# Kernel optimization log

Hardware: AMD Instinct MI355X
Metric: run time of the kernel (lower is better)

## Reference

```python
import jax, jax.numpy as jnp
import numpy as np

S = 8192      # total packed tokens
H = 1152      # hidden size
NH = 16       # heads
HD = 72       # head dim
NSEG = 8      # number of packed (equal-length) sequences
L = S // NSEG # tokens per sequence
SCALE = HD ** -0.5


def setup_inputs() -> dict:
    key = jax.random.key(0)
    ks = jax.random.split(key, 4)
    hidden_states = jax.random.normal(ks[0], (1, S, H), jnp.float32)
    # Real rotary cos/sin per token position within each sequence.
    inv_freq = 1.0 / (10000.0 ** (np.arange(0, HD, 2, dtype=np.float64) / HD))
    freqs = np.outer(np.arange(L, dtype=np.float64), inv_freq)  # [L, HD/2]
    emb = np.concatenate([freqs, freqs], axis=-1)               # [L, HD]
    cos = jnp.asarray(np.tile(np.cos(emb), (NSEG, 1)), jnp.float32)  # [S, HD]
    sin = jnp.asarray(np.tile(np.sin(emb), (NSEG, 1)), jnp.float32)
    Wqkv = jax.random.normal(ks[1], (H, 3 * H), jnp.float32) * (H ** -0.5)
    bqkv = jnp.zeros((3 * H,), jnp.float32)
    Wout = jax.random.normal(ks[2], (H, H), jnp.float32) * (H ** -0.5)
    bout = jnp.zeros((H,), jnp.float32)
    cu_seqlens = jnp.arange(NSEG + 1, dtype=jnp.int32) * L
    return dict(hidden_states=hidden_states, cos=cos, sin=sin,
                Wqkv=Wqkv, bqkv=bqkv, Wout=Wout, bout=bout,
                cu_seqlens=cu_seqlens)


def _rotate_half(x):
    return jnp.concatenate([-x[..., HD // 2:], x[..., :HD // 2]], axis=-1)


def reference(hidden_states, cos, sin, Wqkv, bqkv, Wout, bout, cu_seqlens):
    # QKV projection (fused)
    qkv = hidden_states @ Wqkv + bqkv                 # [1, S, 3H]
    q, k, v = jnp.split(qkv, [H, 2 * H], axis=-1)
    q = q.reshape(1, S, NH, HD)
    k = k.reshape(1, S, NH, HD)
    v = v.reshape(1, S, NH, HD)
    # Inline RoPE on q/k (cos/sin broadcast over heads)
    c = cos[None, :, None, :]
    s = sin[None, :, None, :]
    q = q * c + _rotate_half(q) * s
    k = k * c + _rotate_half(k) * s
    # Varlen (block-diagonal) non-causal attention: equal-length segments
    q = q.reshape(NSEG, L, NH, HD)
    k = k.reshape(NSEG, L, NH, HD)
    v = v.reshape(NSEG, L, NH, HD)
    scores = jnp.einsum('nqhd,nkhd->nhqk', q, k) * SCALE  # [NSEG, NH, L, L]
    probs = jax.nn.softmax(scores, axis=-1)
    ctx = jnp.einsum('nhqk,nkhd->nqhd', probs, v)         # [NSEG, L, NH, HD]
    ctx = ctx.reshape(1, S, H)
    # Output projection
    return ctx @ Wout + bout
```

## Files before the change

kernel.cpp:

```cpp
#include <hip/hip_runtime.h>
#include <hip/hip_fp16.h>
#include <cstdint>

typedef _Float16 half8 __attribute__((ext_vector_type(8)));
typedef _Float16 half4 __attribute__((ext_vector_type(4)));
typedef float floatx4 __attribute__((ext_vector_type(4)));

#define S_TOT 8192
#define H_DIM 1152
#define NHEAD 16
#define HD 72
#define QSTR 96
#define KSTR 104
#define PSTR 76
#define VSTR 76
#define VT_TILE 6080
#define NSEG 8
#define SEGL 1024
#define QSCALE 0.17002324631230988f

__device__ __forceinline__ void gld_lds16(const void* g, void* l) {
  __builtin_amdgcn_global_load_lds((const __attribute__((address_space(1))) void*)g,
                                   (__attribute__((address_space(3))) void*)l, 16, 0, 0);
}

__global__ void cast_f32_f16(const float* __restrict__ in, _Float16* __restrict__ out, int n) {
  int i = (blockIdx.x * 256 + threadIdx.x) * 4;
  if (i < n) {
    float4 v = *(const float4*)(in + i);
    half4 o = { (_Float16)v.x, (_Float16)v.y, (_Float16)v.z, (_Float16)v.w };
    *(half4*)(out + i) = o;
  }
}

__global__ void transpose_cast(const float* __restrict__ W, _Float16* __restrict__ Wt,
                               int R, int C) {
  __shared__ float tile[32][33];
  int tx = threadIdx.x, ty = threadIdx.y;
  int bx = blockIdx.x, by = blockIdx.y;
#pragma unroll
  for (int i = 0; i < 4; ++i)
    tile[ty + i * 8][tx] = W[(size_t)(by * 32 + ty + i * 8) * C + bx * 32 + tx];
  __syncthreads();
#pragma unroll
  for (int i = 0; i < 4; ++i)
    Wt[(size_t)(bx * 32 + ty + i * 8) * R + by * 32 + tx] = (_Float16)tile[tx][ty + i * 8];
}

template <bool OUT_HALF>
__global__ __launch_bounds__(512, 2) void gemm256(
    const _Float16* __restrict__ A, const _Float16* __restrict__ Bt,
    const float* __restrict__ bias, float* __restrict__ Cf, _Float16* __restrict__ Ch,
    int M, int N, int K, int NT) {
  extern __shared__ half8 smem8[];
  char* smem = (char*)smem8;
  const int tid = threadIdx.x;
  const int lane = tid & 63;
  const int w = tid >> 6;
  const int quad = lane >> 4, l16 = lane & 15;
  const int wm = w >> 2, wn = w & 3;

  const int orig = blockIdx.x;
  const int xcd = orig & 7, widx = orig >> 3;
  const int mt = xcd * 4 + (widx & 3), nt = widx >> 2;
  const int m0 = mt * 256, n0 = nt * 256;

  const _Float16* pA[2];
  const _Float16* pB[2];
#pragma unroll
  for (int i = 0; i < 2; ++i) {
    int c = i * 512 + tid;
    int r = c >> 2, cs = c & 3;
    int col = ((cs ^ ((r >> 1) & 3)) << 3);
    pA[i] = A + (size_t)(m0 + r) * K + col;
    int br = n0 + r; if (br >= N) br = N - 1;
    pB[i] = Bt + (size_t)br * K + col;
  }
  const int st0 = tid * 16, st1 = tid * 16 + 8192;
  const int rsl = ((quad ^ ((l16 >> 1) & 3)) << 4);
  const int aoff = (wm * 128 + l16) * 64 + rsl;
  const int boff = 16384 + (wn * 64 + l16) * 64 + rsl;

  half8 afA[8], bfA[4], afB[8], bfB[4];
  floatx4 acc[8][4] = {};

#define STG_A(ds, kcol) { \
  gld_lds16(pA[0] + (kcol), smem + (ds) * 32768 + st0); \
  gld_lds16(pA[1] + (kcol), smem + (ds) * 32768 + st1); }
#define STG_B(ds, kcol) { \
  gld_lds16(pB[0] + (kcol), smem + (ds) * 32768 + 16384 + st0); \
  gld_lds16(pB[1] + (kcol), smem + (ds) * 32768 + 16384 + st1); }
#define LDB4(s, bfx) { \
  _Pragma("unroll") for (int in = 0; in < 4; ++in) \
    bfx[in] = *(const half8*)(smem + (s) * 32768 + boff + in * 1024); }
#define LDA8(s, afx) { \
  _Pragma("unroll") for (int j = 0; j < 8; ++j) \
    afx[j] = *(const half8*)(smem + (s) * 32768 + aoff + j * 1024); }
#define MFMA32(afx, bfx) { \
  __builtin_amdgcn_s_setprio(1); \
  _Pragma("unroll") for (int j = 0; j < 8; ++j) \
  _Pragma("unroll") for (int in = 0; in < 4; ++in) \
    acc[j][in] = \
      __builtin_amdgcn_mfma_f32_16x16x32_f16(afx[j], bfx[in], acc[j][in], 0, 0, 0); \
  __builtin_amdgcn_s_setprio(0); }
#define BAR() __builtin_amdgcn_s_barrier()
#define SBAR() __builtin_amdgcn_sched_barrier(0)
#define LGKM0() { asm volatile("s_waitcnt lgkmcnt(0)" ::: "memory"); SBAR(); }
#define VMWAIT(t) { \
  if ((t) + 3 < KT)        { asm volatile("s_waitcnt vmcnt(4)" ::: "memory"); } \
  else if ((t) + 3 == KT)  { asm volatile("s_waitcnt vmcnt(0)" ::: "memory"); } }

  STG_A(0, 0);  STG_B(0, 0);
  STG_A(1, 32); STG_B(1, 32);
  STG_A(2, 64); STG_B(2, 64);
  asm volatile("s_waitcnt vmcnt(4)" ::: "memory");
  BAR();
  LDB4(0, bfA); LDA8(0, afA);
  LGKM0();

  const int KT = K >> 5;
#pragma unroll 1
  for (int u = 0; u < KT; u += 2) {
    {
      const int rs = (u + 1) & 3, ws = (u + 3) & 3;
      LDB4(rs, bfB); LDA8(rs, afB);
      if (u + 3 < KT) { STG_A(ws, (u + 3) * 32); STG_B(ws, (u + 3) * 32); }
      SBAR();
      MFMA32(afA, bfA);
      SBAR();
      LGKM0();
      VMWAIT(u);
      BAR();
    }
    {
      const int rs = (u + 2) & 3, ws = (u + 4) & 3;
      if (u + 2 < KT) { LDB4(rs, bfA); LDA8(rs, afA); }
      if (u + 4 < KT) { STG_A(ws, (u + 4) * 32); STG_B(ws, (u + 4) * 32); }
      SBAR();
      MFMA32(afB, bfB);
      SBAR();
      LGKM0();
      VMWAIT(u + 1);
      if (u + 2 < KT) BAR();
    }
  }
#undef STG_A
#undef STG_B
#undef LDB4
#undef LDA8
#undef MFMA32
#undef BAR
#undef SBAR
#undef LGKM0
#undef VMWAIT

#pragma unroll
  for (int im = 0; im < 8; ++im) {
    int m = m0 + wm * 128 + im * 16 + quad * 4;
#pragma unroll
    for (int in = 0; in < 4; ++in) {
      int n = n0 + wn * 64 + in * 16 + l16;
      if (n < N) {
        float b = bias[n];
#pragma unroll
        for (int r = 0; r < 4; ++r) {
          float v = acc[im][in][r] + b;
          if (OUT_HALF) Ch[(size_t)(m + r) * N + n] = (_Float16)v;
          else          Cf[(size_t)(m + r) * N + n] = v;
        }
      }
    }
  }
}

template <bool OUT_HALF>
__global__ __launch_bounds__(256) void gemm_bt(
    const _Float16* __restrict__ A, const _Float16* __restrict__ Bt,
    const float* __restrict__ bias, float* __restrict__ Cf, _Float16* __restrict__ Ch,
    int M, int N, int K, int NT) {
  __shared__ __align__(16) _Float16 As[128 * 72];
  __shared__ __align__(16) _Float16 Bs[128 * 72];
  const int tid = threadIdx.x;
  const int lane = tid & 63, w = tid >> 6;
  const int quad = lane >> 4, l16 = lane & 15;
  const int wm = w >> 1, wn = w & 1;
  const int id = blockIdx.x;
  const int j = id & 7, k = id >> 3;
  const int nt_ = k % NT, mt_ = (k / NT) * 8 + j;
  const int m0 = mt_ * 128, n0 = nt_ * 128;

  int rowi[5], cci[5];
#pragma unroll
  for (int i = 0; i < 5; ++i) {
    int c = tid + i * 256;
    int r = c / 9, cc = c - r * 9;
    rowi[i] = r;
    cci[i] = (cc == 8) ? 0 : cc;
  }

  floatx4 acc[4][4] = {};

  for (int kt = 0; kt < K; kt += 64) {
    __syncthreads();
#pragma unroll
    for (int i = 0; i < 4; ++i) {
      gld_lds16(A + (size_t)(m0 + rowi[i]) * K + kt + cci[i] * 8, (char*)As + (tid + i * 256) * 16);
      gld_lds16(Bt + (size_t)(n0 + rowi[i]) * K + kt + cci[i] * 8, (char*)Bs + (tid + i * 256) * 16);
    }
    if (tid < 128) {
      gld_lds16(A + (size_t)(m0 + rowi[4]) * K + kt + cci[4] * 8, (char*)As + (tid + 1024) * 16);
      gld_lds16(Bt + (size_t)(n0 + rowi[4]) * K + kt + cci[4] * 8, (char*)Bs + (tid + 1024) * 16);
    }
    __syncthreads();
#pragma unroll
    for (int kk = 0; kk < 2; ++kk) {
      half8 af[4], bf[4];
#pragma unroll
      for (int im = 0; im < 4; ++im)
        af[im] = *(const half8*)&As[(wm * 64 + im * 16 + l16) * 72 + kk * 32 + quad * 8];
#pragma unroll
      for (int in = 0; in < 4; ++in)
        bf[in] = *(const half8*)&Bs[(wn * 64 + in * 16 + l16) * 72 + kk * 32 + quad * 8];
#pragma unroll
      for (int im = 0; im < 4; ++im)
#pragma unroll
        for (int in = 0; in < 4; ++in)
          acc[im][in] = __builtin_amdgcn_mfma_f32_16x16x32_f16(af[im], bf[in], acc[im][in], 0, 0, 0);
    }
  }
#pragma unroll
  for (int im = 0; im < 4; ++im) {
    int m = m0 + wm * 64 + im * 16 + quad * 4;
#pragma unroll
    for (int in = 0; in < 4; ++in) {
      int n = n0 + wn * 64 + in * 16 + l16;
      float b = bias[n];
#pragma unroll
      for (int r = 0; r < 4; ++r) {
        float v = acc[im][in][r] + b;
        if (OUT_HALF) Ch[(size_t)(m + r) * N + n] = (_Float16)v;
        else          Cf[(size_t)(m + r) * N + n] = v;
      }
    }
  }
}

__global__ __launch_bounds__(256) void rope_scatter(
    const _Float16* __restrict__ QKV,
    const float* __restrict__ cosb,
    const float* __restrict__ sinb,
    _Float16* __restrict__ Qo, _Float16* __restrict__ Ko) {
  __shared__ __align__(16) _Float16 Ls[256 * 120];
  const int tid = threadIdx.x;
  const int t0 = blockIdx.x * 256;
  const int t = t0 + tid;
  const int l = t & 1023, h = (t >> 10) & 15, n = t >> 14;
  const int s = n * SEGL + l;
  const _Float16* q = QKV + (size_t)s * 3456 + h * HD;
  const _Float16* k = q + H_DIM;
  const float* cs = cosb + (size_t)s * HD;
  const float* sn = sinb + (size_t)s * HD;
  half8 z = {};
  {
    _Float16 qr[72], qv[72];
#pragma unroll
    for (int i = 0; i < 9; ++i) *(half8*)&qr[8 * i] = *(const half8*)(q + 8 * i);
#pragma unroll
    for (int d = 0; d < 36; ++d) {
      float c0 = cs[d], s0 = sn[d], c1 = cs[d + 36], s1 = sn[d + 36];
      float a = (float)qr[d], b = (float)qr[d + 36];
      qv[d]      = (_Float16)((a * c0 - b * s0) * QSCALE);
      qv[d + 36] = (_Float16)((b * c1 + a * s1) * QSCALE);
    }
#pragma unroll
    for (int i = 0; i < 9; ++i) *(half8*)&Ls[tid * 104 + 8 * i] = *(half8*)&qv[8 * i];
#pragma unroll
    for (int i = 9; i < 12; ++i) *(half8*)&Ls[tid * 104 + 8 * i] = z;
  }
  __syncthreads();
  {
    _Float16* dst = Qo + (size_t)t0 * QSTR;
#pragma unroll
    for (int it = 0; it < 12; ++it) {
      int j = tid + it * 256;
      int row = j / 12, c = j - row * 12;
      *(half8*)(dst + (size_t)j * 8) = *(const half8*)&Ls[row * 104 + c * 8];
    }
  }
  __syncthreads();
  {
    _Float16 kr[72], kv[72];
#pragma unroll
    for (int i = 0; i < 9; ++i) *(half8*)&kr[8 * i] = *(const half8*)(k + 8 * i);
#pragma unroll
    for (int d = 0; d < 36; ++d) {
      float c0 = cs[d], s0 = sn[d], c1 = cs[d + 36], s1 = sn[d + 36];
      float a = (float)kr[d], b = (float)kr[d + 36];
      kv[d]      = (_Float16)(a * c0 - b * s0);
      kv[d + 36] = (_Float16)(b * c1 + a * s1);
    }
#pragma unroll
    for (int i = 0; i < 9; ++i) *(half8*)&Ls[tid * 120 + 8 * i] = *(half8*)&kv[8 * i];
#pragma unroll
    for (int i = 9; i < 13; ++i) *(half8*)&Ls[tid * 120 + 8 * i] = z;
  }
  __syncthreads();
  {
    _Float16* dst = Ko + (size_t)t0 * KSTR;
#pragma unroll
    for (int it = 0; it < 13; ++it) {
      int j = tid + it * 256;
      int row = j / 13, c = j - row * 13;
      *(half8*)(dst + (size_t)j * 8) = *(const half8*)&Ls[row * 120 + c * 8];
    }
  }
}

__global__ __launch_bounds__(256) void transpose_v(const _Float16* __restrict__ QKV,
                                                   _Float16* __restrict__ Vt) {
  __shared__ __align__(16) _Float16 Vs[64 * 88];
  const int tid = threadIdx.x;
  const int kb = blockIdx.x, h = blockIdx.y, n = blockIdx.z;
  const int s0 = n * SEGL + kb * 64;
  const _Float16* src = QKV + (size_t)s0 * 3456 + 2 * H_DIM + h * HD;
  for (int idx = tid; idx < 576; idx += 256) {
    int key = idx / 9, c = idx - key * 9;
    *(half8*)&Vs[key * 88 + c * 8] = *(const half8*)(src + (size_t)key * 3456 + c * 8);
  }
  __syncthreads();
  _Float16* dst = Vt + (((size_t)(n * NHEAD + h)) * 16 + kb) * VT_TILE;
  for (int idx = tid; idx < 800; idx += 256) {
    int d = idx / 10, c = idx - d * 10;
    if (c < 8) {
      half8 v = {};
      if (d < HD) {
#pragma unroll
        for (int j = 0; j < 8; ++j) v[j] = Vs[(c * 8 + j) * 88 + d];
      } else if (d == HD) {
#pragma unroll
        for (int j = 0; j < 8; ++j) v[j] = (_Float16)1.0f;
      }
      *(half8*)(dst + d * VSTR + c * 8) = v;
    } else if (c == 8) {
      *(half8*)(dst + d * VSTR + 64) = half8{};
    } else {
      *(half4*)(dst + d * VSTR + 72) = half4{};
    }
  }
}

__global__ __launch_bounds__(256, 2) void attn_kernel(
    const _Float16* __restrict__ Qb, const _Float16* __restrict__ Kb,
    const _Float16* __restrict__ Vtb, _Float16* __restrict__ Ctx) {
  extern __shared__ __align__(16) char asmem[];
  const int tid = threadIdx.x;
  const int lane = tid & 63, w = tid >> 6;
  const int quad = lane >> 4, l16 = lane & 15;
  const int id = blockIdx.x;
  const int hn = id & 127, qb = id >> 7;
  const int h = hn >> 3, n = hn & 7;
  const size_t hseg = (size_t)(n * NHEAD + h);
  const _Float16* Qg = Qb + hseg * SEGL * QSTR;
  const _Float16* Kg = Kb + hseg * SEGL * KSTR;
  const _Float16* Vg = Vtb + hseg * 16 * VT_TILE;
  _Float16* Ps = (_Float16*)(asmem + 57344);

  auto STAGE = [&](int kb2, int slot) {
    const char* kbase = (const char*)(Kg + (size_t)kb2 * 64 * KSTR);
    char* kdst = asmem + slot * 28672;
    gld_lds16(kbase + tid * 16,         kdst + tid * 16);
    gld_lds16(kbase + tid * 16 + 4096,  kdst + tid * 16 + 4096);
    gld_lds16(kbase + tid * 16 + 8192,  kdst + tid * 16 + 8192);
    int ko = tid * 16 + 12288; if (ko > 13296) ko = 13296;
    gld_lds16(kbase + ko,               kdst + tid * 16 + 12288);
    const char* vbase = (const char*)(Vg + (size_t)kb2 * VT_TILE);
    char* vdst = kdst + 16384;
    gld_lds16(vbase + tid * 16,         vdst + tid * 16);
    gld_lds16(vbase + tid * 16 + 4096,  vdst + tid * 16 + 4096);
    int vo = tid * 16 + 8192; if (vo > 12144) vo = 12144;
    gld_lds16(vbase + vo,               vdst + tid * 16 + 8192);
  };

  half8 qf[2][3];
#pragma unroll
  for (int qg = 0; qg < 2; ++qg) {
    int row = qb * 128 + w * 32 + qg * 16 + l16;
#pragma unroll
    for (int kc = 0; kc < 3; ++kc)
      qf[qg][kc] = *(const half8*)(Qg + (size_t)row * QSTR + kc * 32 + quad * 8);
  }
  floatx4 o_acc[2][5] = {};

  STAGE(0, 0);
  for (int kb = 0; kb < SEGL / 64; ++kb) {
    __syncthreads();
    if (kb < SEGL / 64 - 1) STAGE(kb + 1, (kb + 1) & 1);
    const _Float16* Kt = (const _Float16*)(asmem + (kb & 1) * 28672);
    const _Float16* Vt = (const _Float16*)(asmem + (kb & 1) * 28672 + 16384);
    floatx4 sa[2][4] = {};
    __builtin_amdgcn_s_setprio(1);
#pragma unroll
    for (int nt = 0; nt < 4; ++nt) {
      half8 kf[3];
#pragma unroll
      for (int kc = 0; kc < 3; ++kc)
        kf[kc] = *(const half8*)&Kt[(nt * 16 + l16) * KSTR + kc * 32 + quad * 8];
#pragma unroll
      for (int qg = 0; qg < 2; ++qg)
#pragma unroll
        for (int kc = 0; kc < 3; ++kc)
          sa[qg][nt] = __builtin_amdgcn_mfma_f32_16x16x32_f16(kf[kc], qf[qg][kc], sa[qg][nt], 0, 0, 0);
    }
    __builtin_amdgcn_s_setprio(0);
#pragma unroll
    for (int qg = 0; qg < 2; ++qg)
#pragma unroll
      for (int nt = 0; nt < 4; ++nt)
#pragma unroll
        for (int r = 0; r < 4; ++r)
          sa[qg][nt][r] = exp2f(sa[qg][nt][r]);
    half8 vf[2][5];
#pragma unroll
    for (int kc2 = 0; kc2 < 2; ++kc2)
#pragma unroll
      for (int t = 0; t < 5; ++t)
        vf[kc2][t] = *(const half8*)&Vt[(t * 16 + l16) * VSTR + kc2 * 32 + quad * 8];
#pragma unroll
    for (int qg = 0; qg < 2; ++qg) {
      int prow = (w * 16 + l16) * PSTR;
#pragma unroll
      for (int nt = 0; nt < 4; ++nt) {
        half4 ph = { (_Float16)sa[qg][nt][0], (_Float16)sa[qg][nt][1],
                     (_Float16)sa[qg][nt][2], (_Float16)sa[qg][nt][3] };
        *(half4*)&Ps[prow + nt * 16 + quad * 4] = ph;
      }
      __builtin_amdgcn_s_setprio(1);
#pragma unroll
      for (int kc2 = 0; kc2 < 2; ++kc2) {
        half8 pb = *(const half8*)&Ps[(w * 16 + l16) * PSTR + kc2 * 32 + quad * 8];
#pragma unroll
        for (int t = 0; t < 5; ++t)
          o_acc[qg][t] = __builtin_amdgcn_mfma_f32_16x16x32_f16(vf[kc2][t], pb, o_acc[qg][t], 0, 0, 0);
      }
      __builtin_amdgcn_s_setprio(0);
    }
  }
#pragma unroll
  for (int qg = 0; qg < 2; ++qg) {
    float lsum = __shfl(o_acc[qg][4][0], 32 + l16, 64);
    float rl = 1.0f / lsum;
    size_t s2 = (size_t)n * SEGL + qb * 128 + w * 32 + qg * 16 + l16;
#pragma unroll
    for (int t = 0; t < 5; ++t) {
      int d0 = t * 16 + quad * 4;
      if (d0 < HD) {
        half4 hv = { (_Float16)(o_acc[qg][t][0] * rl), (_Float16)(o_acc[qg][t][1] * rl),
                     (_Float16)(o_acc[qg][t][2] * rl), (_Float16)(o_acc[qg][t][3] * rl) };
        *(half4*)&Ctx[s2 * H_DIM + h * HD + d0] = hv;
      }
    }
  }
}

extern "C" void kernel_launch(void* const* d_in, const int* in_sizes, int n_in,
                              void* d_out, int out_size, void* d_ws, size_t ws_size,
                              hipStream_t stream) {
  const float* X    = (const float*)d_in[0];
  const float* cosb = (const float*)d_in[1];
  const float* sinb = (const float*)d_in[2];
  const float* Wqkv = (const float*)d_in[3];
  const float* bqkv = (const float*)d_in[4];
  const float* Wout = (const float*)d_in[5];
  const float* bout = (const float*)d_in[6];
  float* out = (float*)d_out;
  char* ws = (char*)d_ws;

  _Float16* Xb   = (_Float16*)(ws);
  _Float16* Wqt  = (_Float16*)(ws + 18874368);
  _Float16* Wot  = (_Float16*)(ws + 26836992);
  _Float16* QKVb = (_Float16*)(ws + 29491200);
  _Float16* Qb   = (_Float16*)(ws + 86114304);
  _Float16* Kb   = (_Float16*)(ws + 111280128);
  _Float16* Vtb  = (_Float16*)(ws + 138543104);
  _Float16* Ctx  = Xb;

  static bool attr_done = false;
  if (!attr_done) {
    hipFuncSetAttribute(reinterpret_cast<const void*>(gemm256<true>),
                        hipFuncAttributeMaxDynamicSharedMemorySize, 131072);
    hipFuncSetAttribute(reinterpret_cast<const void*>(attn_kernel),
                        hipFuncAttributeMaxDynamicSharedMemorySize, 67072);
    attr_done = true;
  }

  cast_f32_f16<<<9216, 256, 0, stream>>>(X, Xb, S_TOT * H_DIM);
  transpose_cast<<<dim3(108, 36), dim3(32, 8), 0, stream>>>(Wqkv, Wqt, H_DIM, 3 * H_DIM);
  transpose_cast<<<dim3(36, 36), dim3(32, 8), 0, stream>>>(Wout, Wot, H_DIM, H_DIM);
  gemm256<true><<<448, 512, 131072, stream>>>(Xb, Wqt, bqkv, nullptr, QKVb,
                                              S_TOT, 3 * H_DIM, H_DIM, 14);
  rope_scatter<<<512, 256, 0, stream>>>(QKVb, cosb, sinb, Qb, Kb);
  transpose_v<<<dim3(16, 16, 8), 256, 0, stream>>>(QKVb, Vtb);
  attn_kernel<<<1024, 256, 67072, stream>>>(Qb, Kb, Vtb, Ctx);
  gemm_bt<false><<<576, 256, 0, stream>>>(Ctx, Wot, bout, out, nullptr,
                                          S_TOT, H_DIM, H_DIM, 9);
}
```

Measured before the change: 419.0 us.

## Single-buffer attention K/V tiles in static LDS to fit three blocks per CU

Replaces the double-buffered async K/V staging in the attention kernel with a single static LDS buffer that is loaded and synchronized inside each iteration. Launch bounds go from 2 to 3 blocks per CU, so LDS per block shrinks to allow higher occupancy. In exchange, the prefetch overlap between loading the next K/V tile and computing the current one is lost. Each iteration now waits on its own load and adds a second barrier, with only other resident blocks left to hide that latency.

```diff
diff --git a/kernel.cpp b/kernel.cpp
--- a/kernel.cpp
+++ b/kernel.cpp
@@ -349,10 +349,12 @@
   }
 }
 
-__global__ __launch_bounds__(256, 2) void attn_kernel(
+__global__ __launch_bounds__(256, 3) void attn_kernel(
     const _Float16* __restrict__ Qb, const _Float16* __restrict__ Kb,
     const _Float16* __restrict__ Vtb, _Float16* __restrict__ Ctx) {
-  extern __shared__ __align__(16) char asmem[];
+  __shared__ __align__(16) _Float16 Kt[64 * KSTR];
+  __shared__ __align__(16) _Float16 Vt[80 * VSTR];
+  __shared__ __align__(16) _Float16 Ps[4 * 16 * PSTR];
   const int tid = threadIdx.x;
   const int lane = tid & 63, w = tid >> 6;
   const int quad = lane >> 4, l16 = lane & 15;
@@ -363,23 +365,6 @@
   const _Float16* Qg = Qb + hseg * SEGL * QSTR;
   const _Float16* Kg = Kb + hseg * SEGL * KSTR;
   const _Float16* Vg = Vtb + hseg * 16 * VT_TILE;
-  _Float16* Ps = (_Float16*)(asmem + 57344);
-
-  auto STAGE = [&](int kb2, int slot) {
-    const char* kbase = (const char*)(Kg + (size_t)kb2 * 64 * KSTR);
-    char* kdst = asmem + slot * 28672;
-    gld_lds16(kbase + tid * 16,         kdst + tid * 16);
-    gld_lds16(kbase + tid * 16 + 4096,  kdst + tid * 16 + 4096);
-    gld_lds16(kbase + tid * 16 + 8192,  kdst + tid * 16 + 8192);
-    int ko = tid * 16 + 12288; if (ko > 13296) ko = 13296;
-    gld_lds16(kbase + ko,               kdst + tid * 16 + 12288);
-    const char* vbase = (const char*)(Vg + (size_t)kb2 * VT_TILE);
-    char* vdst = kdst + 16384;
-    gld_lds16(vbase + tid * 16,         vdst + tid * 16);
-    gld_lds16(vbase + tid * 16 + 4096,  vdst + tid * 16 + 4096);
-    int vo = tid * 16 + 8192; if (vo > 12144) vo = 12144;
-    gld_lds16(vbase + vo,               vdst + tid * 16 + 8192);
-  };
 
   half8 qf[2][3];
 #pragma unroll
@@ -391,12 +376,25 @@
   }
   floatx4 o_acc[2][5] = {};
 
-  STAGE(0, 0);
   for (int kb = 0; kb < SEGL / 64; ++kb) {
     __syncthreads();
-    if (kb < SEGL / 64 - 1) STAGE(kb + 1, (kb + 1) & 1);
-    const _Float16* Kt = (const _Float16*)(asmem + (kb & 1) * 28672);
-    const _Float16* Vt = (const _Float16*)(asmem + (kb & 1) * 28672 + 16384);
+    {
+      const char* base = (const char*)(Kg + (size_t)kb * 64 * KSTR);
+#pragma unroll
+      for (int i = 0; i < 3; ++i)
+        gld_lds16(base + tid * 16 + i * 4096, (char*)Kt + tid * 16 + i * 4096);
+      if (tid < 64)
+        gld_lds16(base + 12288 + tid * 16, (char*)Kt + 12288 + tid * 16);
+    }
+    {
+      const char* base = (const char*)(Vg + (size_t)kb * VT_TILE);
+#pragma unroll
+      for (int i = 0; i < 2; ++i)
+        gld_lds16(base + tid * 16 + i * 4096, (char*)Vt + tid * 16 + i * 4096);
+      if (tid < 248)
+        gld_lds16(base + 8192 + tid * 16, (char*)Vt + 8192 + tid * 16);
+    }
+    __syncthreads();
     floatx4 sa[2][4] = {};
     __builtin_amdgcn_s_setprio(1);
 #pragma unroll
@@ -488,8 +486,6 @@
   if (!attr_done) {
     hipFuncSetAttribute(reinterpret_cast<const void*>(gemm256<true>),
                         hipFuncAttributeMaxDynamicSharedMemorySize, 131072);
-    hipFuncSetAttribute(reinterpret_cast<const void*>(attn_kernel),
-                        hipFuncAttributeMaxDynamicSharedMemorySize, 67072);
     attr_done = true;
   }
 
@@ -500,7 +496,7 @@
                                               S_TOT, 3 * H_DIM, H_DIM, 14);
   rope_scatter<<<512, 256, 0, stream>>>(QKVb, cosb, sinb, Qb, Kb);
   transpose_v<<<dim3(16, 16, 8), 256, 0, stream>>>(QKVb, Vtb);
-  attn_kernel<<<1024, 256, 67072, stream>>>(Qb, Kb, Vtb, Ctx);
+  attn_kernel<<<1024, 256, 0, stream>>>(Qb, Kb, Vtb, Ctx);
   gemm_bt<false><<<576, 256, 0, stream>>>(Ctx, Wot, bout, out, nullptr,
                                           S_TOT, H_DIM, H_DIM, 9);
 }
```

Result: faster. 354.1 us (-15.5%).
